# Kernel optimization log

Hardware: AMD Instinct MI355X
Metric: run time of the kernel (lower is better)

## Reference

```python
import jax, jax.numpy as jnp
import numpy as np

B, T, D_IN, D_H, F = 64, 512, 128, 512, 32


def setup_inputs() -> dict:
    key = jax.random.key(0)
    ks = jax.random.split(key, 8)
    s_in = 1.0 / np.sqrt(D_IN)
    s_h = 1.0 / np.sqrt(D_H)
    return {
        "input_sequence": jax.random.normal(ks[0], (B, T, D_IN), dtype=jnp.float32),
        "Wx0": jax.random.normal(ks[1], (D_H, D_IN), dtype=jnp.float32) * s_in,
        "b0": jnp.zeros((D_H,), dtype=jnp.float32),
        "Wh0": jax.random.normal(ks[2], (D_H, D_H), dtype=jnp.float32) * (0.8 * s_h),
        "d0": jnp.asarray(0.9, dtype=jnp.float32),
        "Wx1": jax.random.normal(ks[3], (D_H, D_H), dtype=jnp.float32) * s_h,
        "b1": jnp.zeros((D_H,), dtype=jnp.float32),
        "Wh1": jax.random.normal(ks[4], (D_H, D_H), dtype=jnp.float32) * (0.8 * s_h),
        "d1": jnp.asarray(0.9, dtype=jnp.float32),
        "Wp": jax.random.normal(ks[5], (D_IN, D_H), dtype=jnp.float32) * s_h,
        "bp": jnp.zeros((D_IN,), dtype=jnp.float32),
        "forecast_steps": F,
    }


def reference(input_sequence, Wx0, b0, Wh0, d0, Wx1, b1, Wh1, d1, Wp, bp, forecast_steps):
    batch = input_sequence.shape[0]
    hdim = Wh0.shape[0]

    def step(h0, h1, x):
        # h_t = decay * W_h h_{t-1} + W_x x_t + b ; layer 1 consumes updated h0
        h0 = d0 * (h0 @ Wh0.T) + x @ Wx0.T + b0
        h1 = d1 * (h1 @ Wh1.T) + h0 @ Wx1.T + b1
        return h0, h1

    # ---- encode context (scan over time, time-major) ----
    xs = jnp.swapaxes(input_sequence, 0, 1)  # [T, B, D_in]
    h0 = jnp.zeros((batch, hdim), dtype=input_sequence.dtype)
    h1 = jnp.zeros((batch, hdim), dtype=input_sequence.dtype)

    def enc(carry, xt):
        return step(*carry, xt), None

    (h0, h1), _ = jax.lax.scan(enc, (h0, h1), xs)

    pred0 = h1 @ Wp.T + bp  # [B, D_in]

    def dec(carry, _):
        h0, h1, p = carry
        h0, h1 = step(h0, h1, p)
        p_new = h1 @ Wp.T + bp
        return (h0, h1, p_new), p_new

    _, rest = jax.lax.scan(dec, (h0, h1, pred0), None, length=forecast_steps - 1)
    forecasts = jnp.concatenate([pred0[None], rest], axis=0)  # [F, B, D_in]
    return jnp.swapaxes(forecasts, 0, 1)  # [B, F, D_in]
```

## Files before the change

kernel.cpp:

```cpp
#include <hip/hip_runtime.h>
#include <cstddef>


typedef _Float16 f16;
typedef _Float16 f16x8 __attribute__((ext_vector_type(8)));
typedef _Float16 f16x4 __attribute__((ext_vector_type(4)));
typedef float f32x4 __attribute__((ext_vector_type(4)));

#define NCTR 32
#define LDA  136
#define ALPHAF 0.00390625f
#define RALPHAF 256.0f
#define DIN 128
#define NF 32

constexpr int SZ = 512*512;
constexpr int off_cat   = 0;
constexpr int off_catA1 = 327680;
constexpr int off_A0c   = 851968;
constexpr int off_A1c   = 1114112;
constexpr int off_Wpr   = 1376256;
constexpr int off_Wpc   = 1441792;
constexpr int off_Gr    = 1507328;
constexpr int off_Gc    = 2555904;
constexpr int off_P0    = 3604480;
constexpr int off_P1    = 5177344;
constexpr int GPr       = 6750208;
constexpr int GPc       = 7798784;
constexpr int GQr       = 8847360;
constexpr int GQc       = 9895936;
constexpr int off_Xin   = 10944512;
constexpr int BA        = 15138816;
constexpr int BB        = 17235968;
constexpr int BC        = 19333120;
constexpr int BD        = 21430272;
constexpr int off_S     = 23527424;
constexpr int off_Dc    = 25624576;
constexpr int off_Db    = 25690112;
constexpr int off_b0h   = 25952256;
constexpr int off_b1h   = 25952768;
constexpr int off_b0ah  = 25953280;
constexpr int off_b1ah  = 25953792;
constexpr int off_bph   = 25954304;
constexpr int off_bpX   = 25954432;
constexpr int off_ctr   = 25962624;

__host__ __device__ constexpr bool dynb(int off){
  return (off >= off_Gr && off < off_Xin) || (off >= BA && off < off_b0h);
}

constexpr int P0r(int s){ return off_P0 + s*524288; }
constexpr int P0c(int s){ return off_P0 + s*524288 + 262144; }
constexpr int P1r(int s){ return off_P1 + s*524288; }
constexpr int P1c(int s){ return off_P1 + s*524288 + 262144; }
constexpr int Bb(int k){ return k==0 ? off_Dc : off_Db + (k-1)*65536; }

struct Op {
  int type;
  int m_off, m_rstride, rows, cols;
  int k1, x1_off, x1_ks, x1_s1, x1_s2;
  int k2, x2_off, x2_ks, x2_s1, x2_s2;
  int add_off, add_ks, add_s1, add_s2;
  int bias_off; float scale;
  int y_off, y_ks, y_s1, y_s2;
  int yt_off, yt_rstride;
  int out32, tile_base;
};
constexpr int MAXOPS = 80, MAXG = 32;
struct Plan { Op ops[MAXOPS]; int gstart[MAXG+1]; int gtiles[MAXG]; int nops, ng; };

constexpr Op mko() {
  Op o{};
  o.type=0; o.m_off=0; o.m_rstride=512; o.rows=512; o.cols=512;
  o.k1=512; o.x1_off=0; o.x1_ks=512; o.x1_s1=64; o.x1_s2=0;
  o.k2=0; o.x2_off=0; o.x2_ks=512; o.x2_s1=64; o.x2_s2=0;
  o.add_off=-1; o.add_ks=512; o.add_s1=64; o.add_s2=0;
  o.bias_off=-1; o.scale=1.0f;
  o.y_off=-1; o.y_ks=512; o.y_s1=64; o.y_s2=0;
  o.yt_off=-1; o.yt_rstride=512; o.out32=0; o.tile_base=0;
  return o;
}
constexpr int op_ntiles(const Op& o){ return (o.rows>>6)*(o.cols>>6); }

struct Builder { Plan p{}; int nops=0, ng=0, gtile=0; };
constexpr void push(Builder& b, Op o){ o.tile_base=b.gtile; b.gtile+=op_ntiles(o); b.p.ops[b.nops++]=o; }
constexpr void endg(Builder& b){ b.p.gtiles[b.ng]=b.gtile; b.ng++; b.p.gstart[b.ng]=b.nops; b.gtile=0; }

constexpr Op SQ2(int m,int mrs,int x1c,int yc,int yr){
  Op o=mko(); o.m_off=m; o.m_rstride=mrs; o.x1_off=x1c; o.y_off=yc; o.yt_off=yr; return o; }
constexpr Op SQG(int mr,int xc,int yc,int yr){
  Op o=mko(); o.rows=1024; o.cols=1024; o.k1=1024; o.m_off=mr; o.m_rstride=1024;
  o.x1_off=xc; o.x1_ks=1024; o.y_off=yc; o.y_ks=1024; o.yt_off=yr; o.yt_rstride=1024; return o; }
constexpr Op P2S(int s){
  Op o=mko(); o.cols=4096; o.bias_off=off_b0h;
  o.k2=128; o.x2_off=off_Xin; o.x2_ks=128; o.x2_s1=512; o.x2_s2=(s-1)*64;
  o.y_off=(s&1)?BA:BB;
  if (s==1){ o.m_off=off_cat+512; o.m_rstride=640; o.k1=0; }
  else { o.m_off=off_cat; o.m_rstride=640; o.k1=512; o.x1_off=(s&1)?BB:BA; }
  return o; }
constexpr Op HS(int s){
  Op o=mko(); o.m_off=off_cat; o.m_rstride=640; o.cols=4096;
  o.k1=512; o.x1_off=(s&1)?BC:BB;
  o.k2=128; o.x2_off=off_Xin; o.x2_ks=128; o.x2_s1=512; o.x2_s2=(s-1)*64;
  o.bias_off=off_b0h; o.y_off=(s&1)?BB:BC; return o; }
constexpr Op RS(int s){
  Op o=mko(); o.cols=4096; o.bias_off=off_b1h;
  if (s==1){ o.m_off=off_catA1+512; o.m_rstride=1024; o.k1=512; o.x1_off=BB; o.y_off=BD; }
  else { o.m_off=off_catA1; o.m_rstride=1024; o.k1=512; o.x1_off=(s&1)?BA:BD;
         o.k2=512; o.x2_off=(s&1)?BB:BC; o.x2_ks=512; o.x2_s1=64; o.x2_s2=0;
         o.y_off=(s&1)?BD:BA; }
  return o; }
constexpr Op SCAN(int m,int d,int inb,int outb){
  Op o=mko(); o.m_off=m; o.cols=4096-d*64; o.x1_off=inb;
  o.add_off=inb; o.add_s2=d*64; o.y_off=outb; o.y_s2=d*64; return o; }
constexpr Op SCOPY(int d,int inb,int outb){
  Op o=mko(); o.k1=0; o.cols=d*64; o.add_off=inb; o.y_off=outb; return o; }
constexpr Op FOLDL(int m,int cols,int inb,int outb){
  Op o=mko(); o.m_off=m; o.cols=cols; o.x1_off=inb; o.x1_s1=128;
  o.add_off=inb; o.add_s1=128; o.add_s2=64; o.y_off=outb; return o; }
constexpr Op DECA(int k,int moff){
  Op o=mko(); int m=1<<k;
  o.rows=1024; o.cols=m*64; o.k1=1024; o.m_off=moff; o.m_rstride=1024;
  o.x1_off=off_S; o.x1_ks=1024; o.bias_off=Bb(k);
  o.y_off=off_S; o.y_ks=1024; o.y_s2=m*64; return o; }
constexpr Op DECB(int k,int moff){
  Op o=mko(); o.rows=1024; o.cols=64; o.k1=1024; o.m_off=moff; o.m_rstride=1024;
  o.x1_off=Bb(k); o.x1_ks=1024; o.bias_off=Bb(k);
  o.y_off=Bb(k+1); o.y_ks=1024; return o; }

constexpr Plan build_plan() {
  Builder b{}; b.p.gstart[0]=0;
  push(b, SQ2(off_cat,640,off_A0c,P0c(0),P0r(0)));
  push(b, SQ2(off_catA1,1024,off_A1c,P1c(0),P1r(0)));
  { Op o=mko(); o.m_off=off_cat+512; o.m_rstride=640; o.k1=128; o.x1_off=off_Wpc; o.x1_ks=128;
    o.y_off=off_Gc+512*1024; o.y_ks=1024; o.yt_off=off_Gr+512; o.yt_rstride=1024; push(b,o); }
  { Op o=mko(); o.m_off=off_cat+512; o.m_rstride=640; o.k1=128; o.x1_off=off_bpX; o.x1_ks=128;
    o.cols=64; o.bias_off=off_b0ah; o.scale=ALPHAF; o.y_off=off_Dc; o.y_ks=1024; push(b,o); }
  push(b, P2S(1)); endg(b);
  push(b, SQ2(P0r(0),512,P0c(0),P0c(1),P0r(1)));
  push(b, SQ2(P1r(0),512,P1c(0),P1c(1),P1r(1)));
  { Op o=mko(); o.m_off=off_catA1+512; o.m_rstride=1024; o.x1_off=off_A0c;
    o.y_off=off_Gc+512; o.y_ks=1024; o.yt_off=off_Gr+512*1024; o.yt_rstride=1024; push(b,o); }
  { Op o=mko(); o.m_off=off_catA1+512; o.m_rstride=1024; o.x1_off=off_Dc; o.x1_ks=1024;
    o.cols=64; o.bias_off=off_b1ah; o.y_off=off_Dc+512; o.y_ks=1024; push(b,o); }
  push(b, P2S(2)); endg(b);
  push(b, SQ2(P0r(1),512,P0c(1),P0c(2),P0r(2)));
  push(b, SQ2(P1r(1),512,P1c(1),P1c(2),P1r(2)));
  { Op o=mko(); o.m_off=off_catA1+512; o.m_rstride=1024; o.x1_off=off_Gc+512*1024; o.x1_ks=1024;
    o.add_off=off_A1c; o.y_off=off_Gc+512*1024+512; o.y_ks=1024;
    o.yt_off=off_Gr+512*1024+512; o.yt_rstride=1024; push(b,o); }
  push(b, P2S(3)); endg(b);
  push(b, SQ2(P0r(2),512,P0c(2),P0c(0),P0r(0)));
  push(b, SQ2(P1r(2),512,P1c(2),P1c(0),P1r(0)));
  push(b, P2S(4)); endg(b);
  push(b, SQ2(P0r(0),512,P0c(0),P0c(1),P0r(1)));
  push(b, SQ2(P1r(0),512,P1c(0),P1c(1),P1r(1)));
  push(b, P2S(5)); endg(b);
  push(b, P2S(6));
  push(b, SQG(off_Gr, off_Gc, GPc, GPr)); endg(b);
  push(b, P2S(7)); endg(b);
  push(b, P2S(8)); endg(b);
  push(b, SCAN(P0r(2), 1, BB, BA)); push(b, SCOPY(1, BB, BA)); endg(b);
  push(b, SCAN(P0r(0), 2, BA, BB)); push(b, SCOPY(2, BA, BB)); endg(b);
  push(b, SCAN(P0r(1), 4, BB, BA)); push(b, SCOPY(4, BB, BA)); endg(b);
  { Op o=mko(); o.m_off=off_cat; o.m_rstride=640; o.cols=4032; o.k1=512; o.x1_off=BA;
    o.k2=128; o.x2_off=off_Xin; o.x2_ks=128; o.x2_s1=512; o.x2_s2=512;
    o.bias_off=off_b0h; o.y_off=BB; o.y_s2=64; push(b,o); }
  { Op o=mko(); o.m_off=off_cat+512; o.m_rstride=640; o.cols=64; o.k1=0;
    o.k2=128; o.x2_off=off_Xin; o.x2_ks=128; o.x2_s1=512; o.x2_s2=0;
    o.bias_off=off_b0h; o.y_off=BB; push(b,o); }
  endg(b);
  for (int s=1; s<=7; ++s){ push(b, HS(s+1)); push(b, RS(s)); endg(b); }
  push(b, RS(8));
  { Op o=mko(); o.k1=0; o.cols=64; o.add_off=BC; o.add_s2=4032; o.scale=ALPHAF;
    o.y_off=off_S; o.y_ks=1024; push(b,o); }
  endg(b);
  push(b, FOLDL(P1r(2), 2048, BA, BB)); endg(b);
  push(b, FOLDL(P1r(0), 1024, BB, BC)); endg(b);
  { Op o=mko(); o.m_off=P1r(1); o.cols=64; o.x1_off=BC; o.x1_s2=896;
    o.add_off=BC; o.add_s2=960; o.scale=ALPHAF;
    o.y_off=off_S+512; o.y_ks=1024; push(b,o); }
  endg(b);
  push(b, DECA(0, off_Gr)); push(b, DECB(0, off_Gr)); endg(b);
  push(b, DECA(1, GPr)); push(b, DECB(1, GPr)); push(b, SQG(GPr,GPc,GQc,GQr)); endg(b);
  push(b, DECA(2, GQr)); push(b, DECB(2, GQr)); push(b, SQG(GQr,GQc,GPc,GPr)); endg(b);
  push(b, DECA(3, GPr)); push(b, DECB(3, GPr)); push(b, SQG(GPr,GPc,GQc,GQr)); endg(b);
  push(b, DECA(4, GQr)); endg(b);
  { Op o=mko(); o.m_off=off_Wpr; o.rows=128; o.cols=2048; o.x1_off=off_S+512; o.x1_ks=1024;
    o.bias_off=off_bph; o.scale=RALPHAF; o.out32=1; push(b,o); }
  endg(b);
  b.p.nops=b.nops; b.p.ng=b.ng;
  return b.p;
}
static constexpr Plan h_plan = build_plan();
__device__ __constant__ Plan d_plan = h_plan;

__device__ inline void issue4(const f16* p, f16x8 (&r)[4], bool cc) {
  if (cc)
    asm volatile(
      "global_load_dwordx4 %0, %4, off sc0 sc1\n\t"
      "global_load_dwordx4 %1, %4, off offset:16 sc0 sc1\n\t"
      "global_load_dwordx4 %2, %4, off offset:32 sc0 sc1\n\t"
      "global_load_dwordx4 %3, %4, off offset:48 sc0 sc1"
      : "=&v"(r[0]), "=&v"(r[1]), "=&v"(r[2]), "=&v"(r[3])
      : "v"(p) : "memory");
  else
    asm volatile(
      "global_load_dwordx4 %0, %4, off\n\t"
      "global_load_dwordx4 %1, %4, off offset:16\n\t"
      "global_load_dwordx4 %2, %4, off offset:32\n\t"
      "global_load_dwordx4 %3, %4, off offset:48"
      : "=&v"(r[0]), "=&v"(r[1]), "=&v"(r[2]), "=&v"(r[3])
      : "v"(p) : "memory");
}
__device__ inline void issue_ld8(const f16* p, f16x4& r) {
  asm volatile("global_load_dwordx2 %0, %1, off sc0 sc1"
               : "=&v"(r) : "v"(p) : "memory");
}
__device__ inline void st8_cc(f16* p, f16x4 v) {
  asm volatile("global_store_dwordx2 %0, %1, off sc0 sc1" :: "v"(p), "v"(v) : "memory");
}
__device__ inline void st2_cc(f16* p, f16 v) {
  unsigned d = __builtin_bit_cast(unsigned short, v);
  asm volatile("global_store_short %0, %1, off sc0 sc1" :: "v"(p), "v"(d) : "memory");
}
__device__ inline unsigned ld_u32_cc(const unsigned* p) {
  unsigned r;
  asm volatile("global_load_dword %0, %1, off sc0 sc1\n\ts_waitcnt vmcnt(0)"
               : "=&v"(r) : "v"(p) : "memory");
  return r;
}
__device__ inline void st_u32_cc(unsigned* p, unsigned v) {
  asm volatile("global_store_dword %0, %1, off sc0 sc1" :: "v"(p), "v"(v) : "memory");
}

__device__ inline void grid_barrier(unsigned* ctrs, unsigned* flag, unsigned epoch) {
  __syncthreads();
  if (threadIdx.x == 0)
    __hip_atomic_fetch_add(&ctrs[(blockIdx.x & (NCTR-1))*32], 1u,
                           __ATOMIC_RELAXED, __HIP_MEMORY_SCOPE_AGENT);
  if (blockIdx.x == 0) {
    if (threadIdx.x < NCTR) {
      const unsigned tgt = epoch * (gridDim.x / NCTR);
      while (ld_u32_cc(&ctrs[threadIdx.x*32]) < tgt)
        __builtin_amdgcn_s_sleep(2);
    }
    __syncthreads();
    if (threadIdx.x == 0) st_u32_cc(flag, epoch);
  } else if (threadIdx.x == 0) {
    while (ld_u32_cc(flag) < epoch)
      __builtin_amdgcn_s_sleep(2);
  }
  __syncthreads();
}

__device__ inline void chunk_srcs(const Op& o, const f16* w, int r0, int c0, int kc,
                                  const f16*& pa, const f16*& pb, bool& bcc) {
  const int tid = threadIdx.x;
  pa = w + o.m_off + (size_t)(r0 + (tid>>2)) * o.m_rstride + kc + (tid&3)*32;
  int C = c0 + (tid>>2);
  int xo, xks, xs1, xs2, xk;
  if (kc < o.k1) { xo=o.x1_off; xks=o.x1_ks; xs1=o.x1_s1; xs2=o.x1_s2; xk=kc; }
  else           { xo=o.x2_off; xks=o.x2_ks; xs1=o.x2_s1; xs2=o.x2_s2; xk=kc-o.k1; }
  int xcol = xs1*(C>>6) + (C&63) + xs2;
  pb = w + xo + (size_t)xcol*xks + xk + (tid&3)*32;
  bcc = dynb(xo);
}

__device__ inline void st_lds(f16* lsA, f16* lsB, const f16x8 (&ra)[4], const f16x8 (&rb)[4]) {
  const int tid = threadIdx.x;
  f16* da = lsA + (tid>>2)*LDA + (tid&3)*32;
#pragma unroll
  for (int i=0;i<4;++i) *(f16x8*)(da + i*8) = ra[i];
  f16* db = lsB + (tid>>2)*LDA + (tid&3)*32;
#pragma unroll
  for (int i=0;i<4;++i) *(f16x8*)(db + i*8) = rb[i];
}

__device__ inline void mfma_lds(const f16* lsA, const f16* lsB, f32x4 (&acc)[4]) {
  const int tid = threadIdx.x, lane = tid & 63, wid = tid >> 6;
  const int ko = (lane >> 4) * 8, rl = lane & 15;
#pragma unroll
  for (int kb = 0; kb < 4; ++kb) {
    f16x8 a = *(const f16x8*)(lsA + (wid*16 + rl) * LDA + kb*32 + ko);
#pragma unroll
    for (int n = 0; n < 4; ++n) {
      f16x8 bb = *(const f16x8*)(lsB + (n*16 + rl) * LDA + kb*32 + ko);
      acc[n] = __builtin_amdgcn_mfma_f32_16x16x32_f16(a, bb, acc[n], 0, 0, 0);
    }
  }
}

#define CH_STEP(c_, raX, rbX)                                                  \
  do {                                                                         \
    __syncthreads();                                                           \
    if ((c_) < nch - 1) asm volatile("s_waitcnt vmcnt(8)" ::: "memory");       \
    else                asm volatile("s_waitcnt vmcnt(0)" ::: "memory");       \
    st_lds(lsA, lsB, raX, rbX);                                                \
    __syncthreads();                                                           \
    if ((c_) + 2 < nch) {                                                      \
      chunk_srcs(o, w, r0, c0, ((c_)+2)*128, pa, pb, bcc);                     \
      issue4(pa, raX, mcc); issue4(pb, rbX, bcc);                              \
    }                                                                          \
    mfma_lds(lsA, lsB, acc);                                                   \
  } while (0)

__device__ void run_tile(const Op& o, int local, f16* w, float* out, f16* lsA, f16* lsB) {
  int nct = o.cols >> 6;
  int rg = local / nct, ct = local - rg * nct;
  int r0 = rg << 6, c0 = ct << 6;
  const bool mcc = dynb(o.m_off);
  const bool addcc = dynb(o.add_off);
  const bool biascc = dynb(o.bias_off);
  f32x4 acc[4];
#pragma unroll
  for (int n=0;n<4;++n) acc[n] = f32x4{0.f,0.f,0.f,0.f};
  int nch = (o.k1 + o.k2) >> 7;
  if (nch > 0) {
    const f16 *pa, *pb; bool bcc;
    f16x8 ra0[4], rb0[4], ra1[4], rb1[4];
    chunk_srcs(o, w, r0, c0, 0, pa, pb, bcc);
    issue4(pa, ra0, mcc); issue4(pb, rb0, bcc);
    if (nch > 1) {
      chunk_srcs(o, w, r0, c0, 128, pa, pb, bcc);
      issue4(pa, ra1, mcc); issue4(pb, rb1, bcc);
    }
    for (int c = 0; c < nch; c += 2) {
      CH_STEP(c, ra0, rb0);
      if (c + 1 < nch) CH_STEP(c+1, ra1, rb1);
    }
  }
  const int tid = threadIdx.x, lane = tid & 63, wid = tid >> 6;
  const int q4 = (lane >> 4) * 4, cl = lane & 15;
  const int r = r0 + wid*16 + q4;
  f16x4 addv[4], biasv;
  bool pend = false;
  if (o.add_off >= 0) {
#pragma unroll
    for (int n = 0; n < 4; ++n) {
      int C = c0 + n*16 + cl;
      int acol = o.add_s1 * (C>>6) + (C&63) + o.add_s2;
      const f16* ap = w + o.add_off + (size_t)acol * o.add_ks + r;
      if (addcc) { issue_ld8(ap, addv[n]); pend = true; }
      else addv[n] = *(const f16x4*)ap;
    }
  }
  if (o.bias_off >= 0) {
    const f16* bp2 = w + o.bias_off + r;
    if (biascc) { issue_ld8(bp2, biasv); pend = true; }
    else biasv = *(const f16x4*)bp2;
  }
  if (pend) asm volatile("s_waitcnt vmcnt(0)" ::: "memory");
#pragma unroll
  for (int n = 0; n < 4; ++n) {
    int C = c0 + n*16 + cl;
    f32x4 v = acc[n];
    if (o.add_off >= 0) {
      v[0]+=(float)addv[n][0]; v[1]+=(float)addv[n][1];
      v[2]+=(float)addv[n][2]; v[3]+=(float)addv[n][3];
    }
    v[0]*=o.scale; v[1]*=o.scale; v[2]*=o.scale; v[3]*=o.scale;
    if (o.bias_off >= 0) {
      v[0]+=(float)biasv[0]; v[1]+=(float)biasv[1];
      v[2]+=(float)biasv[2]; v[3]+=(float)biasv[3];
    }
    if (o.y_off >= 0) {
      int ycol = o.y_s1 * (C>>6) + (C&63) + o.y_s2;
      f16* yp = w + o.y_off + (size_t)ycol * o.y_ks + r;
      f16x4 h; h[0]=(f16)v[0]; h[1]=(f16)v[1]; h[2]=(f16)v[2]; h[3]=(f16)v[3];
      st8_cc(yp, h);
    }
    if (o.yt_off >= 0) {
      f16* tp = w + o.yt_off;
      st2_cc(tp + (size_t)(r+0)*o.yt_rstride + C, (f16)v[0]);
      st2_cc(tp + (size_t)(r+1)*o.yt_rstride + C, (f16)v[1]);
      st2_cc(tp + (size_t)(r+2)*o.yt_rstride + C, (f16)v[2]);
      st2_cc(tp + (size_t)(r+3)*o.yt_rstride + C, (f16)v[3]);
    }
    if (o.out32) {
      float* op2 = out + (size_t)(C & 63) * (NF*DIN) + (size_t)(C >> 6) * DIN + r;
      op2[0]=v[0]; op2[1]=v[1]; op2[2]=v[2]; op2[3]=v[3];
    }
  }
}

__global__ __launch_bounds__(256, 2) void rnn_main(f16* w, float* out) {
  __shared__ f16 lsA[64*LDA];
  __shared__ f16 lsB[64*LDA];
  unsigned* ctrs = (unsigned*)(w + off_ctr);
  unsigned* flag = ctrs + NCTR*32;
  const int wg = blockIdx.x;
  const int stride = gridDim.x;
  const int ng = d_plan.ng;
  for (int g = 0; g < ng; ++g) {
    int o0 = d_plan.gstart[g], o1 = d_plan.gstart[g+1];
    int gtot = d_plan.gtiles[g];
    for (int t = wg; t < gtot; t += stride) {
      int oi = o0;
      while (oi + 1 < o1 && t >= d_plan.ops[oi+1].tile_base) ++oi;
      run_tile(d_plan.ops[oi], t - d_plan.ops[oi].tile_base, w, out, lsA, lsB);
    }
    grid_barrier(ctrs, flag, (unsigned)(g + 1));
  }
}

__global__ void rnn_prep(f16* w, const float* X, const float* Wx0, const float* b0,
    const float* Wh0, const float* d0p, const float* Wx1, const float* b1,
    const float* Wh1, const float* d1p, const float* Wp, const float* bp)
{
  const float d0 = d0p[0], d1 = d1p[0];
  const long n0=512L*640, n1=512L*1024, n2=(long)SZ, n3=(long)SZ, n4=128L*512, n5=512L*128,
             n6=(long)SZ, n7=(long)SZ, n8=32768L*128, n9=512, n10=512, n11=512, n12=512,
             n13=128, n14=64L*128, n15=2048;
  const long total = n0+n1+n2+n3+n4+n5+n6+n7+n8+n9+n10+n11+n12+n13+n14+n15;
  for (long idx = (long)blockIdx.x*blockDim.x + threadIdx.x; idx < total;
       idx += (long)gridDim.x*blockDim.x) {
    long j = idx;
    if (j < n0) { int r=(int)(j/640), c=(int)(j%640);
      w[off_cat+j] = (f16)(c<512 ? d0*Wh0[(long)r*512+c] : Wx0[(long)r*128+(c-512)]); continue; }
    j -= n0;
    if (j < n1) { int r=(int)(j>>10), c=(int)(j&1023);
      w[off_catA1+j] = (f16)(c<512 ? d1*Wh1[(long)r*512+c] : Wx1[(long)r*512+(c-512)]); continue; }
    j -= n1;
    if (j < n2) { int c=(int)(j>>9), r=(int)(j&511); w[off_A0c+j] = (f16)(d0*Wh0[(long)r*512+c]); continue; }
    j -= n2;
    if (j < n3) { int c=(int)(j>>9), r=(int)(j&511); w[off_A1c+j] = (f16)(d1*Wh1[(long)r*512+c]); continue; }
    j -= n3;
    if (j < n4) { w[off_Wpr+j] = (f16)Wp[j]; continue; }
    j -= n4;
    if (j < n5) { int c=(int)(j>>7), k=(int)(j&127); w[off_Wpc+j] = (f16)Wp[(long)k*512+c]; continue; }
    j -= n5;
    if (j < n6) { int r=(int)(j>>9), c=(int)(j&511);
      w[off_Gr + (long)r*1024 + c] = (f16)(d0*Wh0[(long)r*512+c]); continue; }
    j -= n6;
    if (j < n7) { int c=(int)(j>>9), r=(int)(j&511);
      w[off_Gc + (long)c*1024 + r] = (f16)(d0*Wh0[(long)r*512+c]); continue; }
    j -= n7;
    if (j < n8) { int col=(int)(j>>7), d=(int)(j&127); int t=col>>6, bb=col&63;
      w[off_Xin+j] = (f16)X[((long)bb<<16) + ((long)t<<7) + d]; continue; }
    j -= n8;
    if (j < n9) { w[off_b0h+j] = (f16)b0[j]; continue; }  j -= n9;
    if (j < n10){ w[off_b1h+j] = (f16)b1[j]; continue; }  j -= n10;
    if (j < n11){ w[off_b0ah+j] = (f16)(ALPHAF*b0[j]); continue; }  j -= n11;
    if (j < n12){ w[off_b1ah+j] = (f16)(ALPHAF*b1[j]); continue; }  j -= n12;
    if (j < n13){ w[off_bph+j] = (f16)bp[j]; continue; }  j -= n13;
    if (j < n14){ int k=(int)(j&127); w[off_bpX+j] = (f16)bp[k]; continue; }  j -= n14;
    ((unsigned*)(w + off_ctr))[j] = 0u;
  }
}

extern "C" void kernel_launch(void* const* d_in, const int* in_sizes, int n_in,
                              void* d_out, int out_size, void* d_ws, size_t ws_size,
                              hipStream_t stream) {
  (void)in_sizes; (void)n_in; (void)out_size; (void)ws_size;
  f16* w = (f16*)d_ws;
  hipLaunchKernelGGL(rnn_prep, dim3(2048), dim3(256), 0, stream,
      w,
      (const float*)d_in[0], (const float*)d_in[1], (const float*)d_in[2],
      (const float*)d_in[3], (const float*)d_in[4], (const float*)d_in[5],
      (const float*)d_in[6], (const float*)d_in[7], (const float*)d_in[8],
      (const float*)d_in[9], (const float*)d_in[10]);
  float* outp = (float*)d_out;
  void* kargs[] = { (void*)&w, (void*)&outp };
  int nb = 0;
  hipError_t qe = hipOccupancyMaxActiveBlocksPerMultiprocessor(
      &nb, (const void*)rnn_main, 256, 0);
  int grid = (qe == hipSuccess && nb >= 2) ? 512 : 256;
  hipError_t le = hipLaunchCooperativeKernel((const void*)rnn_main, dim3(grid),
                                             dim3(256), kargs, 0, stream);
  if (le != hipSuccess && grid == 512) {
    hipLaunchCooperativeKernel((const void*)rnn_main, dim3(256),
                               dim3(256), kargs, 0, stream);
  }
}
```

Measured before the change: 553.9 us.

## Halve tile width to 64x32, triple-buffer loads, raise occupancy and distribute barrier flags

Output tiles shrink from 64x64 to 64x32, which doubles the tile count per group, halves B-operand loads and LDS, and lets launch bounds allow four blocks per CU. The grid grows to up to 1024 cooperative blocks to spread each latency-bound recurrence step over more CUs. Global loads move from two to three chunks in flight, with waitcnt thresholds adjusted to match. The grid barrier release now writes one flag per counter slot instead of a single shared flag, to reduce polling contention. The cost is more A-matrix re-reads per output, fewer MFMAs per tile, and more blocks taking part in each barrier.

Result: slower. 583.0 us (+5.3%).

```diff
diff --git a/kernel.cpp b/kernel.cpp
--- a/kernel.cpp
+++ b/kernel.cpp
@@ -80,7 +80,7 @@
   o.yt_off=-1; o.yt_rstride=512; o.out32=0; o.tile_base=0;
   return o;
 }
-constexpr int op_ntiles(const Op& o){ return (o.rows>>6)*(o.cols>>6); }
+constexpr int op_ntiles(const Op& o){ return (o.rows>>6)*(o.cols>>5); }
 
 struct Builder { Plan p{}; int nops=0, ng=0, gtile=0; };
 constexpr void push(Builder& b, Op o){ o.tile_base=b.gtile; b.gtile+=op_ntiles(o); b.p.ops[b.nops++]=o; }
@@ -195,7 +195,7 @@
 static constexpr Plan h_plan = build_plan();
 __device__ __constant__ Plan d_plan = h_plan;
 
-__device__ inline void issue4(const f16* p, f16x8 (&r)[4], bool cc) {
+__device__ inline void issueA4(const f16* p, f16x8 (&r)[4], bool cc) {
   if (cc)
     asm volatile(
       "global_load_dwordx4 %0, %4, off sc0 sc1\n\t"
@@ -213,6 +213,18 @@
       : "=&v"(r[0]), "=&v"(r[1]), "=&v"(r[2]), "=&v"(r[3])
       : "v"(p) : "memory");
 }
+__device__ inline void issueB2(const f16* p, f16x8 (&r)[2], bool cc) {
+  if (cc)
+    asm volatile(
+      "global_load_dwordx4 %0, %2, off sc0 sc1\n\t"
+      "global_load_dwordx4 %1, %2, off offset:16 sc0 sc1"
+      : "=&v"(r[0]), "=&v"(r[1]) : "v"(p) : "memory");
+  else
+    asm volatile(
+      "global_load_dwordx4 %0, %2, off\n\t"
+      "global_load_dwordx4 %1, %2, off offset:16"
+      : "=&v"(r[0]), "=&v"(r[1]) : "v"(p) : "memory");
+}
 __device__ inline void issue_ld8(const f16* p, f16x4& r) {
   asm volatile("global_load_dwordx2 %0, %1, off sc0 sc1"
                : "=&v"(r) : "v"(p) : "memory");
@@ -234,7 +246,7 @@
   asm volatile("global_store_dword %0, %1, off sc0 sc1" :: "v"(p), "v"(v) : "memory");
 }
 
-__device__ inline void grid_barrier(unsigned* ctrs, unsigned* flag, unsigned epoch) {
+__device__ inline void grid_barrier(unsigned* ctrs, unsigned epoch) {
   __syncthreads();
   if (threadIdx.x == 0)
     __hip_atomic_fetch_add(&ctrs[(blockIdx.x & (NCTR-1))*32], 1u,
@@ -246,10 +258,12 @@
         __builtin_amdgcn_s_sleep(2);
     }
     __syncthreads();
-    if (threadIdx.x == 0) st_u32_cc(flag, epoch);
+    if (threadIdx.x < NCTR)
+      st_u32_cc(&ctrs[(NCTR + threadIdx.x)*32], epoch);
   } else if (threadIdx.x == 0) {
-    while (ld_u32_cc(flag) < epoch)
-      __builtin_amdgcn_s_sleep(2);
+    const unsigned fl = (NCTR + (blockIdx.x & (NCTR-1)))*32;
+    while (ld_u32_cc(&ctrs[fl]) < epoch)
+      __builtin_amdgcn_s_sleep(4);
   }
   __syncthreads();
 }
@@ -258,33 +272,33 @@
                                   const f16*& pa, const f16*& pb, bool& bcc) {
   const int tid = threadIdx.x;
   pa = w + o.m_off + (size_t)(r0 + (tid>>2)) * o.m_rstride + kc + (tid&3)*32;
-  int C = c0 + (tid>>2);
+  int C = c0 + (tid>>3);
   int xo, xks, xs1, xs2, xk;
   if (kc < o.k1) { xo=o.x1_off; xks=o.x1_ks; xs1=o.x1_s1; xs2=o.x1_s2; xk=kc; }
   else           { xo=o.x2_off; xks=o.x2_ks; xs1=o.x2_s1; xs2=o.x2_s2; xk=kc-o.k1; }
   int xcol = xs1*(C>>6) + (C&63) + xs2;
-  pb = w + xo + (size_t)xcol*xks + xk + (tid&3)*32;
+  pb = w + xo + (size_t)xcol*xks + xk + (tid&7)*16;
   bcc = dynb(xo);
 }
 
-__device__ inline void st_lds(f16* lsA, f16* lsB, const f16x8 (&ra)[4], const f16x8 (&rb)[4]) {
+__device__ inline void st_lds(f16* lsA, f16* lsB, const f16x8 (&ra)[4], const f16x8 (&rb)[2]) {
   const int tid = threadIdx.x;
   f16* da = lsA + (tid>>2)*LDA + (tid&3)*32;
 #pragma unroll
   for (int i=0;i<4;++i) *(f16x8*)(da + i*8) = ra[i];
-  f16* db = lsB + (tid>>2)*LDA + (tid&3)*32;
-#pragma unroll
-  for (int i=0;i<4;++i) *(f16x8*)(db + i*8) = rb[i];
-}
-
-__device__ inline void mfma_lds(const f16* lsA, const f16* lsB, f32x4 (&acc)[4]) {
+  f16* db = lsB + (tid>>3)*LDA + (tid&7)*16;
+#pragma unroll
+  for (int i=0;i<2;++i) *(f16x8*)(db + i*8) = rb[i];
+}
+
+__device__ inline void mfma_lds(const f16* lsA, const f16* lsB, f32x4 (&acc)[2]) {
   const int tid = threadIdx.x, lane = tid & 63, wid = tid >> 6;
   const int ko = (lane >> 4) * 8, rl = lane & 15;
 #pragma unroll
   for (int kb = 0; kb < 4; ++kb) {
     f16x8 a = *(const f16x8*)(lsA + (wid*16 + rl) * LDA + kb*32 + ko);
 #pragma unroll
-    for (int n = 0; n < 4; ++n) {
+    for (int n = 0; n < 2; ++n) {
       f16x8 bb = *(const f16x8*)(lsB + (n*16 + rl) * LDA + kb*32 + ko);
       acc[n] = __builtin_amdgcn_mfma_f32_16x16x32_f16(a, bb, acc[n], 0, 0, 0);
     }
@@ -294,50 +308,52 @@
 #define CH_STEP(c_, raX, rbX)                                                  \
   do {                                                                         \
     __syncthreads();                                                           \
-    if ((c_) < nch - 1) asm volatile("s_waitcnt vmcnt(8)" ::: "memory");       \
-    else                asm volatile("s_waitcnt vmcnt(0)" ::: "memory");       \
+    int rem_ = nch - 1 - (c_);                                                 \
+    if (rem_ >= 2)      asm volatile("s_waitcnt vmcnt(12)" ::: "memory");      \
+    else if (rem_ == 1) asm volatile("s_waitcnt vmcnt(6)"  ::: "memory");      \
+    else                asm volatile("s_waitcnt vmcnt(0)"  ::: "memory");      \
     st_lds(lsA, lsB, raX, rbX);                                                \
     __syncthreads();                                                           \
-    if ((c_) + 2 < nch) {                                                      \
-      chunk_srcs(o, w, r0, c0, ((c_)+2)*128, pa, pb, bcc);                     \
-      issue4(pa, raX, mcc); issue4(pb, rbX, bcc);                              \
+    if ((c_) + 3 < nch) {                                                      \
+      chunk_srcs(o, w, r0, c0, ((c_)+3)*128, pa, pb, bcc);                     \
+      issueA4(pa, raX, mcc); issueB2(pb, rbX, bcc);                            \
     }                                                                          \
     mfma_lds(lsA, lsB, acc);                                                   \
   } while (0)
 
 __device__ void run_tile(const Op& o, int local, f16* w, float* out, f16* lsA, f16* lsB) {
-  int nct = o.cols >> 6;
+  int nct = o.cols >> 5;
   int rg = local / nct, ct = local - rg * nct;
-  int r0 = rg << 6, c0 = ct << 6;
+  int r0 = rg << 6, c0 = ct << 5;
   const bool mcc = dynb(o.m_off);
   const bool addcc = dynb(o.add_off);
   const bool biascc = dynb(o.bias_off);
-  f32x4 acc[4];
-#pragma unroll
-  for (int n=0;n<4;++n) acc[n] = f32x4{0.f,0.f,0.f,0.f};
+  f32x4 acc[2];
+  acc[0] = f32x4{0.f,0.f,0.f,0.f}; acc[1] = f32x4{0.f,0.f,0.f,0.f};
   int nch = (o.k1 + o.k2) >> 7;
   if (nch > 0) {
     const f16 *pa, *pb; bool bcc;
-    f16x8 ra0[4], rb0[4], ra1[4], rb1[4];
+    f16x8 ra0[4], rb0[2], ra1[4], rb1[2], ra2[4], rb2[2];
     chunk_srcs(o, w, r0, c0, 0, pa, pb, bcc);
-    issue4(pa, ra0, mcc); issue4(pb, rb0, bcc);
-    if (nch > 1) {
-      chunk_srcs(o, w, r0, c0, 128, pa, pb, bcc);
-      issue4(pa, ra1, mcc); issue4(pb, rb1, bcc);
-    }
-    for (int c = 0; c < nch; c += 2) {
+    issueA4(pa, ra0, mcc); issueB2(pb, rb0, bcc);
+    if (nch > 1) { chunk_srcs(o, w, r0, c0, 128, pa, pb, bcc);
+                   issueA4(pa, ra1, mcc); issueB2(pb, rb1, bcc); }
+    if (nch > 2) { chunk_srcs(o, w, r0, c0, 256, pa, pb, bcc);
+                   issueA4(pa, ra2, mcc); issueB2(pb, rb2, bcc); }
+    for (int c = 0; c < nch; c += 3) {
       CH_STEP(c, ra0, rb0);
       if (c + 1 < nch) CH_STEP(c+1, ra1, rb1);
+      if (c + 2 < nch) CH_STEP(c+2, ra2, rb2);
     }
   }
   const int tid = threadIdx.x, lane = tid & 63, wid = tid >> 6;
   const int q4 = (lane >> 4) * 4, cl = lane & 15;
   const int r = r0 + wid*16 + q4;
-  f16x4 addv[4], biasv;
+  f16x4 addv[2], biasv;
   bool pend = false;
   if (o.add_off >= 0) {
 #pragma unroll
-    for (int n = 0; n < 4; ++n) {
+    for (int n = 0; n < 2; ++n) {
       int C = c0 + n*16 + cl;
       int acol = o.add_s1 * (C>>6) + (C&63) + o.add_s2;
       const f16* ap = w + o.add_off + (size_t)acol * o.add_ks + r;
@@ -352,7 +368,7 @@
   }
   if (pend) asm volatile("s_waitcnt vmcnt(0)" ::: "memory");
 #pragma unroll
-  for (int n = 0; n < 4; ++n) {
+  for (int n = 0; n < 2; ++n) {
     int C = c0 + n*16 + cl;
     f32x4 v = acc[n];
     if (o.add_off >= 0) {
@@ -384,11 +400,10 @@
   }
 }
 
-__global__ __launch_bounds__(256, 2) void rnn_main(f16* w, float* out) {
+__global__ __launch_bounds__(256, 4) void rnn_main(f16* w, float* out) {
   __shared__ f16 lsA[64*LDA];
-  __shared__ f16 lsB[64*LDA];
+  __shared__ f16 lsB[32*LDA];
   unsigned* ctrs = (unsigned*)(w + off_ctr);
-  unsigned* flag = ctrs + NCTR*32;
   const int wg = blockIdx.x;
   const int stride = gridDim.x;
   const int ng = d_plan.ng;
@@ -400,7 +415,7 @@
       while (oi + 1 < o1 && t >= d_plan.ops[oi+1].tile_base) ++oi;
       run_tile(d_plan.ops[oi], t - d_plan.ops[oi].tile_base, w, out, lsA, lsB);
     }
-    grid_barrier(ctrs, flag, (unsigned)(g + 1));
+    grid_barrier(ctrs, (unsigned)(g + 1));
   }
 }
 
@@ -465,11 +480,12 @@
   int nb = 0;
   hipError_t qe = hipOccupancyMaxActiveBlocksPerMultiprocessor(
       &nb, (const void*)rnn_main, 256, 0);
-  int grid = (qe == hipSuccess && nb >= 2) ? 512 : 256;
-  hipError_t le = hipLaunchCooperativeKernel((const void*)rnn_main, dim3(grid),
-                                             dim3(256), kargs, 0, stream);
-  if (le != hipSuccess && grid == 512) {
-    hipLaunchCooperativeKernel((const void*)rnn_main, dim3(256),
-                               dim3(256), kargs, 0, stream);
-  }
-}
+  int bpc = (qe == hipSuccess && nb >= 1) ? (nb >= 4 ? 4 : (nb >= 2 ? 2 : 1)) : 1;
+  int grid = 256 * bpc;
+  while (true) {
+    hipError_t le = hipLaunchCooperativeKernel((const void*)rnn_main, dim3(grid),
+                                               dim3(256), kargs, 0, stream);
+    if (le == hipSuccess || grid <= 256) break;
+    grid >>= 1;
+  }
+}
```
